# Optimization experiments

Hardware: AMD Instinct MI355X
Metric: run time of the kernel (lower is better)

Reference implementation:

```python
import jax, jax.numpy as jnp
import numpy as np

B, S, D, H, F, E = 4, 1024, 1024, 16, 4096, 8
HD = D // H  # head dim


def setup_inputs() -> dict:
    key = jax.random.key(0)
    ks = jax.random.split(key, 8)
    p = lambda k, shp: jax.random.normal(k, shp, jnp.float32) * 0.02
    return {
        "x": jax.random.normal(ks[0], (B, S, D), jnp.float32),
        "mask": jnp.ones((B, S), jnp.int32),
        "in_proj_w": p(ks[1], (3 * D, D)),
        "in_proj_b": jnp.zeros((3 * D,), jnp.float32),
        "out_proj_w": p(ks[2], (D, D)),
        "out_proj_b": jnp.zeros((D,), jnp.float32),
        "ln1_g": jnp.ones((D,), jnp.float32),
        "ln1_b": jnp.zeros((D,), jnp.float32),
        "ln2_g": jnp.ones((D,), jnp.float32),
        "ln2_b": jnp.zeros((D,), jnp.float32),
        "gate_w": p(ks[3], (E, D)),
        "gate_b": jnp.zeros((E,), jnp.float32),
        "w1": p(ks[4], (E, F, D)),
        "b1": jnp.zeros((E, F), jnp.float32),
        "w2": p(ks[5], (E, D, F)),
        "b2": jnp.zeros((E, D), jnp.float32),
    }


def _layernorm(x, g, b, eps=1e-5):
    m = x.mean(-1, keepdims=True)
    v = ((x - m) ** 2).mean(-1, keepdims=True)
    return (x - m) / jnp.sqrt(v + eps) * g + b


def _mha(x, key_pad, in_proj_w, in_proj_b, out_proj_w, out_proj_b):
    # combined QKV projection as in torch nn.MultiheadAttention
    qkv = x @ in_proj_w.T + in_proj_b  # (B,S,3D)
    q, k, v = jnp.split(qkv, 3, axis=-1)
    def heads(t):
        return t.reshape(B, S, H, HD).transpose(0, 2, 1, 3)  # (B,H,S,HD)
    q, k, v = heads(q), heads(k), heads(v)
    scores = jnp.einsum("bhqd,bhkd->bhqk", q, k) / jnp.sqrt(jnp.float32(HD))
    scores = jnp.where(key_pad[:, None, None, :], -1e30, scores)
    attn = jax.nn.softmax(scores, axis=-1)
    out = jnp.einsum("bhqk,bhkd->bhqd", attn, v)  # (B,H,S,HD)
    out = out.transpose(0, 2, 1, 3).reshape(B, S, D)
    return out @ out_proj_w.T + out_proj_b


def _moe(x, gate_w, gate_b, w1, b1, w2, b2):
    logits = x @ gate_w.T + gate_b            # (B,S,E)
    probs = jax.nn.softmax(logits, axis=-1)
    # dense all-expert FFN (faithful to original: every expert computed)
    h = jax.nn.relu(jnp.einsum("bsd,efd->bsef", x, w1) + b1)   # (B,S,E,F)
    all_out = jnp.einsum("bsef,edf->bsed", h, w2) + b2          # (B,S,E,D)
    top_vals, top_idx = jax.lax.top_k(probs, 2)                 # (B,S,2)
    weights = top_vals / (top_vals.sum(-1, keepdims=True) + 1e-9)
    sel = jnp.take_along_axis(all_out, top_idx[..., None], axis=2)  # (B,S,2,D)
    return (sel * weights[..., None]).sum(axis=2)


def reference(x, mask, in_proj_w, in_proj_b, out_proj_w, out_proj_b,
              ln1_g, ln1_b, ln2_g, ln2_b, gate_w, gate_b, w1, b1, w2, b2):
    key_pad = mask == 0  # (B,S) bool
    attn_out = _mha(x, key_pad, in_proj_w, in_proj_b, out_proj_w, out_proj_b)
    x1 = _layernorm(x + attn_out, ln1_g, ln1_b)
    ff = _moe(x1, gate_w, gate_b, w1, b1, w2, b2)
    return _layernorm(x1 + ff, ln2_g, ln2_b)
```

## Files before the change

kernel.cpp:

```cpp
#include <hip/hip_runtime.h>

typedef __attribute__((ext_vector_type(8))) short bf16x8;
typedef __attribute__((ext_vector_type(4))) float f32x4;

#define DEV __device__ __forceinline__

static constexpr int Bb = 4, Sq = 1024, Dd = 1024, Hh = 16, HDd = 64, Ff = 4096, Ee = 8;
static constexpr int Nn = Bb * Sq;
static constexpr int TD = 3 * Dd;
static constexpr int PMAX = 2 * Nn + Ee * 256;

DEV unsigned short f2bf(float x) {
  union { float f; unsigned u; } c; c.f = x;
  unsigned r = c.u + 0x7FFFu + ((c.u >> 16) & 1u);
  return (unsigned short)(r >> 16);
}

typedef const __attribute__((address_space(1))) unsigned int* gas_t;
typedef __attribute__((address_space(3))) unsigned int* las_t;
DEV void gload16(const void* g, void* l) {
  __builtin_amdgcn_global_load_lds((gas_t)g, (las_t)l, 16, 0, 0);
}

__global__ __launch_bounds__(256) void cvt_kernel(const float* __restrict__ in,
                                                  unsigned short* __restrict__ out) {
  int i = blockIdx.x * 256 + threadIdx.x;
  const float4 a = *(const float4*)(in + (size_t)i * 8);
  const float4 b = *(const float4*)(in + (size_t)i * 8 + 4);
  union { uint4 u; unsigned short s[8]; } pk;
  pk.s[0] = f2bf(a.x); pk.s[1] = f2bf(a.y); pk.s[2] = f2bf(a.z); pk.s[3] = f2bf(a.w);
  pk.s[4] = f2bf(b.x); pk.s[5] = f2bf(b.y); pk.s[6] = f2bf(b.z); pk.s[7] = f2bf(b.w);
  *(uint4*)(out + (size_t)i * 8) = pk.u;
}

template <int EPI, int TN>
__global__ __launch_bounds__(512) void gemm256(
    const unsigned short* __restrict__ A, const unsigned short* __restrict__ Bw,
    const float* __restrict__ bias, void* __restrict__ o0,
    int Ncols, int K, const int* __restrict__ poff) {
  constexpr int NW_N = TN / 64;
  constexpr int NW_M = 8 / NW_N;
  constexpr int RM = 256 / NW_M;
  constexpr int MI = RM / 16;
  constexpr int NB = TN / 64;
  constexpr int ASZ = 256 * 64;
  constexpr int BSZ = TN * 64;

  int bx, by;
  {
    const int gx = gridDim.x, nwg = gx * gridDim.y;
    int orig = blockIdx.y * gx + blockIdx.x;
    int q = nwg >> 3, r = nwg & 7;
    int xcd = orig & 7, lin = orig >> 3;
    int wg = (xcd < r ? xcd * (q + 1) : r * (q + 1) + (xcd - r) * q) + lin;
    bx = wg % gx; by = wg / gx;
  }
  const int m0 = bx * 256;
  if (m0 >= poff[Ee]) return;
  int e = 0;
#pragma unroll
  for (int k = 1; k < Ee; ++k) if (m0 >= poff[k]) e = k;
  const int n0 = by * TN;
  const unsigned short* Bptr = Bw + (size_t)e * Ncols * K;
  const float* biasptr = bias + e * Ncols;

  __shared__ __align__(128) unsigned short As[2 * ASZ];
  __shared__ __align__(128) unsigned short Bs[2 * BSZ];

  const int tid = threadIdx.x;
  const int lane = tid & 63, wid = tid >> 6;
  const int wm = wid / NW_N, wn = wid % NW_N;
  const int lr = lane & 15, lk = lane >> 4;

  const char* aSrc[4]; const char* bSrc[NB];
  int aDstOff[4], bDstOff[NB];
#pragma unroll
  for (int it = 0; it < 4; ++it) {
    int b = it * 8192 + tid * 16;
    int r = b >> 7;
    int colb = (b & 127) ^ ((r & 7) << 4);
    aSrc[it] = (const char*)(A + (size_t)(m0 + r) * K) + colb;
    aDstOff[it] = it * 8192 + wid * 1024;
  }
#pragma unroll
  for (int it = 0; it < NB; ++it) {
    int b = it * 8192 + tid * 16;
    int r = b >> 7;
    int colb = (b & 127) ^ ((r & 7) << 4);
    bSrc[it] = (const char*)(Bptr + (size_t)(n0 + r) * K) + colb;
    bDstOff[it] = it * 8192 + wid * 1024;
  }
  int aOff[2][MI], bOff[2][4];
#pragma unroll
  for (int ks = 0; ks < 2; ++ks) {
#pragma unroll
    for (int i = 0; i < MI; ++i) {
      int ra = wm * RM + i * 16 + lr;
      aOff[ks][i] = ra * 64 + (((ks * 4 + lk) ^ (ra & 7)) << 3);
    }
#pragma unroll
    for (int i = 0; i < 4; ++i) {
      int rb = wn * 64 + i * 16 + lr;
      bOff[ks][i] = rb * 64 + (((ks * 4 + lk) ^ (rb & 7)) << 3);
    }
  }

  f32x4 acc[MI][4] = {};
  const int NT = K >> 6;

  auto STAGE = [&](int t, int buf) {
#pragma unroll
    for (int it = 0; it < 4; ++it)
      gload16(aSrc[it] + (size_t)t * 128, (char*)As + buf * (ASZ * 2) + aDstOff[it]);
#pragma unroll
    for (int it = 0; it < NB; ++it)
      gload16(bSrc[it] + (size_t)t * 128, (char*)Bs + buf * (BSZ * 2) + bDstOff[it]);
  };

  STAGE(0, 0);
  for (int t = 0; t < NT; ++t) {
    __builtin_amdgcn_s_barrier();
    __builtin_amdgcn_sched_barrier(0);
    if (t + 1 < NT) {
      STAGE(t + 1, (t + 1) & 1);
      if constexpr (TN == 256) asm volatile("s_waitcnt vmcnt(8)" ::: "memory");
      else                     asm volatile("s_waitcnt vmcnt(6)" ::: "memory");
    } else {
      asm volatile("s_waitcnt vmcnt(0)" ::: "memory");
    }
    __builtin_amdgcn_sched_barrier(0);
    __builtin_amdgcn_s_barrier();
    __builtin_amdgcn_sched_barrier(0);
    const unsigned short* Ab = As + (t & 1) * ASZ;
    const unsigned short* Bb2 = Bs + (t & 1) * BSZ;
#pragma unroll
    for (int ks = 0; ks < 2; ++ks) {
      bf16x8 af[MI], bfv[4];
#pragma unroll
      for (int mi = 0; mi < MI; ++mi) af[mi] = *(const bf16x8*)&Ab[aOff[ks][mi]];
#pragma unroll
      for (int ni = 0; ni < 4; ++ni) bfv[ni] = *(const bf16x8*)&Bb2[bOff[ks][ni]];
#pragma unroll
      for (int mi = 0; mi < MI; ++mi)
#pragma unroll
        for (int ni = 0; ni < 4; ++ni)
          acc[mi][ni] = __builtin_amdgcn_mfma_f32_16x16x32_bf16(af[mi], bfv[ni], acc[mi][ni], 0, 0, 0);
    }
  }

#pragma unroll
  for (int ni = 0; ni < 4; ++ni) {
    const int col = n0 + wn * 64 + ni * 16 + lr;
    const float bv = biasptr[col];
#pragma unroll
    for (int mi = 0; mi < MI; ++mi) {
#pragma unroll
      for (int i = 0; i < 4; ++i) {
        const int grow = m0 + wm * RM + mi * 16 + lk * 4 + i;
        float v = acc[mi][ni][i] + bv;
        if constexpr (EPI == 2) {
          ((unsigned short*)o0)[(size_t)grow * Ff + col] = f2bf(fmaxf(v, 0.f));
        } else {
          ((float*)o0)[(size_t)grow * Dd + col] = v;
        }
      }
    }
  }
}

template <int EPI>
__global__ __launch_bounds__(256) void gemm_bt(
    const unsigned short* __restrict__ A, const unsigned short* __restrict__ Bw,
    const float* __restrict__ bias, void* __restrict__ o0, void* __restrict__ o1,
    void* __restrict__ o2, int M, int Ncols, int K) {
  int bx, by;
  {
    const int gx = gridDim.x, nwg = gx * gridDim.y;
    int orig = blockIdx.y * gx + blockIdx.x;
    int q = nwg >> 3, r = nwg & 7;
    int xcd = orig & 7, lin = orig >> 3;
    int wg = (xcd < r ? xcd * (q + 1) : r * (q + 1) + (xcd - r) * q) + lin;
    bx = wg % gx; by = wg / gx;
  }
  const int m0 = bx * 128;
  if (m0 >= M) return;
  const int n0 = by * 128;

  __shared__ __align__(128) unsigned short As[3 * 128 * 32];
  __shared__ __align__(128) unsigned short Bs[3 * 128 * 32];

  const int tid = threadIdx.x;
  const int lane = tid & 63, wid = tid >> 6;
  const int wm = wid >> 1, wn = wid & 1;
  const int lr = lane & 15, lk = lane >> 4;

  const char* aSrc[2]; const char* bSrc[2];
  int dOff[2];
#pragma unroll
  for (int it = 0; it < 2; ++it) {
    int b = it * 4096 + tid * 16;
    int r = b >> 6;
    int colb = (b & 63) ^ (((r >> 1) & 3) << 4);
    aSrc[it] = (const char*)(A + (size_t)(m0 + r) * K) + colb;
    bSrc[it] = (const char*)(Bw + (size_t)(n0 + r) * K) + colb;
    dOff[it] = it * 4096 + wid * 1024;
  }
  int aOff[4], bOff[4];
#pragma unroll
  for (int i = 0; i < 4; ++i) {
    int ra = wm * 64 + i * 16 + lr;
    aOff[i] = ra * 32 + ((lk ^ ((ra >> 1) & 3)) << 3);
    int rb = wn * 64 + i * 16 + lr;
    bOff[i] = rb * 32 + ((lk ^ ((rb >> 1) & 3)) << 3);
  }

  auto STAGE = [&](int t, int buf) {
#pragma unroll
    for (int it = 0; it < 2; ++it) {
      gload16(aSrc[it] + (size_t)t * 64, (char*)As + buf * 8192 + dOff[it]);
      gload16(bSrc[it] + (size_t)t * 64, (char*)Bs + buf * 8192 + dOff[it]);
    }
  };

  f32x4 acc[4][4] = {};
  const int NT = K >> 5;

  STAGE(0, 0);
  STAGE(1, 1);
  int cb = 0, sb = 2;
  for (int t = 0; t < NT; ++t) {
    if (t + 1 < NT) asm volatile("s_waitcnt vmcnt(4)" ::: "memory");
    else            asm volatile("s_waitcnt vmcnt(0)" ::: "memory");
    __builtin_amdgcn_sched_barrier(0);
    __builtin_amdgcn_s_barrier();
    __builtin_amdgcn_sched_barrier(0);
    if (t + 2 < NT) STAGE(t + 2, sb);
    const unsigned short* Ab = As + cb * 4096;
    const unsigned short* Bb2 = Bs + cb * 4096;
    bf16x8 af[4], bfv[4];
#pragma unroll
    for (int mi = 0; mi < 4; ++mi) af[mi] = *(const bf16x8*)&Ab[aOff[mi]];
#pragma unroll
    for (int ni = 0; ni < 4; ++ni) bfv[ni] = *(const bf16x8*)&Bb2[bOff[ni]];
#pragma unroll
    for (int mi = 0; mi < 4; ++mi)
#pragma unroll
      for (int ni = 0; ni < 4; ++ni)
        acc[mi][ni] = __builtin_amdgcn_mfma_f32_16x16x32_bf16(af[mi], bfv[ni], acc[mi][ni], 0, 0, 0);
    cb = (cb == 2) ? 0 : cb + 1;
    sb = (sb == 2) ? 0 : sb + 1;
  }

#pragma unroll
  for (int ni = 0; ni < 4; ++ni) {
    const int col = n0 + wn * 64 + ni * 16 + lr;
    const float bv = bias[col];
#pragma unroll
    for (int mi = 0; mi < 4; ++mi) {
#pragma unroll
      for (int i = 0; i < 4; ++i) {
        const int mloc = wm * 64 + mi * 16 + lk * 4 + i;
        float v = acc[mi][ni][i] + bv;
        if constexpr (EPI == 0) {
          int t = m0 + mloc;
          int which = col >> 10, jj = col & 1023, hh = jj >> 6, hd = jj & 63;
          int bb = t >> 10, s = t & 1023;
          unsigned short* dst = (which == 0) ? (unsigned short*)o0
                              : (which == 1) ? (unsigned short*)o1 : (unsigned short*)o2;
          dst[((size_t)(bb * Hh + hh) * Sq + s) * HDd + hd] = f2bf(v);
        } else {
          ((float*)o0)[(size_t)(m0 + mloc) * Dd + col] = v;
        }
      }
    }
  }
}

__global__ __launch_bounds__(256) void attn_kernel(
    const unsigned short* __restrict__ qb, const unsigned short* __restrict__ kb,
    const unsigned short* __restrict__ vb, const int* __restrict__ mask,
    unsigned short* __restrict__ attnb) {
  const int qt = blockIdx.x, h = blockIdx.y, b = blockIdx.z;
  const unsigned short* Q = qb + (size_t)(b * Hh + h) * Sq * HDd;
  const unsigned short* Kg = kb + (size_t)(b * Hh + h) * Sq * HDd;
  const unsigned short* Vg = vb + (size_t)(b * Hh + h) * Sq * HDd;

  __shared__ unsigned short Qs[64 * 72], Ks[64 * 72], Vt[64 * 72], Ps[64 * 72];
  __shared__ float Ssm[64 * 65];
  __shared__ float mS[64], lS[64], aS[64];
  __shared__ int mk[64];

  const int tid = threadIdx.x, lane = tid & 63, wid = tid >> 6;
  const int lr = lane & 15, lk = lane >> 4;

#pragma unroll
  for (int it = 0; it < 2; ++it) {
    int c = tid + it * 256; int r = c >> 3, kc = (c & 7) * 8;
    *(uint4*)&Qs[r * 72 + kc] = *(const uint4*)(Q + (size_t)(qt * 64 + r) * 64 + kc);
  }
  if (tid < 64) { mS[tid] = -1e30f; lS[tid] = 0.f; }

  f32x4 oacc[4] = {};

  for (int kt = 0; kt < 16; ++kt) {
    __syncthreads();
#pragma unroll
    for (int it = 0; it < 2; ++it) {
      int c = tid + it * 256; int r = c >> 3, kc = (c & 7) * 8;
      *(uint4*)&Ks[r * 72 + kc] = *(const uint4*)(Kg + (size_t)(kt * 64 + r) * 64 + kc);
    }
    {
      int kk = tid >> 2, hg = (tid & 3) * 16;
      union { uint4 u[2]; unsigned short s[16]; } tv;
      tv.u[0] = *(const uint4*)(Vg + (size_t)(kt * 64 + kk) * 64 + hg);
      tv.u[1] = *(const uint4*)(Vg + (size_t)(kt * 64 + kk) * 64 + hg + 8);
#pragma unroll
      for (int j = 0; j < 16; ++j) Vt[(hg + j) * 72 + kk] = tv.s[j];
    }
    if (tid < 64) mk[tid] = mask[b * Sq + kt * 64 + tid];
    __syncthreads();

    f32x4 sacc[4] = {};
#pragma unroll
    for (int ks = 0; ks < 2; ++ks) {
      bf16x8 aq = *(const bf16x8*)&Qs[(wid * 16 + lr) * 72 + ks * 32 + lk * 8];
#pragma unroll
      for (int ni = 0; ni < 4; ++ni) {
        bf16x8 bk = *(const bf16x8*)&Ks[(ni * 16 + lr) * 72 + ks * 32 + lk * 8];
        sacc[ni] = __builtin_amdgcn_mfma_f32_16x16x32_bf16(aq, bk, sacc[ni], 0, 0, 0);
      }
    }
#pragma unroll
    for (int ni = 0; ni < 4; ++ni)
#pragma unroll
      for (int i = 0; i < 4; ++i) {
        int r = wid * 16 + lk * 4 + i, cc = ni * 16 + lr;
        float v = sacc[ni][i] * 0.125f;
        if (mk[cc] == 0) v = -1e30f;
        Ssm[r * 65 + cc] = v;
      }
    __syncthreads();
    {
      int r = tid >> 2, cg = (tid & 3) * 16;
      float xv[16];
#pragma unroll
      for (int j = 0; j < 16; ++j) xv[j] = Ssm[r * 65 + cg + j];
      float mx = xv[0];
#pragma unroll
      for (int j = 1; j < 16; ++j) mx = fmaxf(mx, xv[j]);
      mx = fmaxf(mx, __shfl_xor(mx, 1));
      mx = fmaxf(mx, __shfl_xor(mx, 2));
      float mprev = mS[r];
      float mnew = fmaxf(mprev, mx);
      float sum = 0.f;
      union { uint4 u[2]; unsigned short s[16]; } pb;
#pragma unroll
      for (int j = 0; j < 16; ++j) {
        float pv = expf(xv[j] - mnew);
        sum += pv; pb.s[j] = f2bf(pv);
      }
      sum += __shfl_xor(sum, 1);
      sum += __shfl_xor(sum, 2);
      *(uint4*)&Ps[r * 72 + cg] = pb.u[0];
      *(uint4*)&Ps[r * 72 + cg + 8] = pb.u[1];
      if ((tid & 3) == 0) {
        float alpha = expf(mprev - mnew);
        mS[r] = mnew; aS[r] = alpha; lS[r] = lS[r] * alpha + sum;
      }
    }
    __syncthreads();
#pragma unroll
    for (int ni = 0; ni < 4; ++ni)
#pragma unroll
      for (int i = 0; i < 4; ++i)
        oacc[ni][i] *= aS[wid * 16 + lk * 4 + i];
#pragma unroll
    for (int ks = 0; ks < 2; ++ks) {
      bf16x8 ap = *(const bf16x8*)&Ps[(wid * 16 + lr) * 72 + ks * 32 + lk * 8];
#pragma unroll
      for (int ni = 0; ni < 4; ++ni) {
        bf16x8 bv = *(const bf16x8*)&Vt[(ni * 16 + lr) * 72 + ks * 32 + lk * 8];
        oacc[ni] = __builtin_amdgcn_mfma_f32_16x16x32_bf16(ap, bv, oacc[ni], 0, 0, 0);
      }
    }
  }
  __syncthreads();
#pragma unroll
  for (int ni = 0; ni < 4; ++ni)
#pragma unroll
    for (int i = 0; i < 4; ++i) {
      int r = wid * 16 + lk * 4 + i;
      int q = qt * 64 + r;
      float v = oacc[ni][i] / lS[r];
      attnb[((size_t)(b * Sq + q)) * Dd + h * 64 + ni * 16 + lr] = f2bf(v);
    }
}

__global__ __launch_bounds__(256) void ln_kernel(
    const float* __restrict__ a, const float* __restrict__ b2,
    const float* __restrict__ g, const float* __restrict__ beta,
    float* __restrict__ outf, unsigned short* __restrict__ outb) {
  const int t = blockIdx.x, tid = threadIdx.x;
  float4 v = *(const float4*)(a + (size_t)t * Dd + tid * 4);
  {
    float4 u = *(const float4*)(b2 + (size_t)t * Dd + tid * 4);
    v.x += u.x; v.y += u.y; v.z += u.z; v.w += u.w;
  }
  const int lane = tid & 63, wid = tid >> 6;
  float s = v.x + v.y + v.z + v.w;
  for (int sh = 1; sh < 64; sh <<= 1) s += __shfl_xor(s, sh);
  __shared__ float red[4], red2[4];
  if (lane == 0) red[wid] = s;
  __syncthreads();
  float mean = (red[0] + red[1] + red[2] + red[3]) * (1.f / Dd);
  float dx = v.x - mean, dy = v.y - mean, dz = v.z - mean, dw = v.w - mean;
  float q = dx * dx + dy * dy + dz * dz + dw * dw;
  for (int sh = 1; sh < 64; sh <<= 1) q += __shfl_xor(q, sh);
  if (lane == 0) red2[wid] = q;
  __syncthreads();
  float var = (red2[0] + red2[1] + red2[2] + red2[3]) * (1.f / Dd);
  float rstd = rsqrtf(var + 1e-5f);
  float4 gg = *(const float4*)(g + tid * 4);
  float4 bb = *(const float4*)(beta + tid * 4);
  float4 o;
  o.x = dx * rstd * gg.x + bb.x;
  o.y = dy * rstd * gg.y + bb.y;
  o.z = dz * rstd * gg.z + bb.z;
  o.w = dw * rstd * gg.w + bb.w;
  if (outf) *(float4*)(outf + (size_t)t * Dd + tid * 4) = o;
  if (outb) {
    ushort4 pk; pk.x = f2bf(o.x); pk.y = f2bf(o.y); pk.z = f2bf(o.z); pk.w = f2bf(o.w);
    *(ushort4*)(outb + (size_t)t * Dd + tid * 4) = pk;
  }
}

__global__ __launch_bounds__(256) void ln2_kernel(
    const float* __restrict__ x1f, const float* __restrict__ ffp,
    const int* __restrict__ inv, const float* __restrict__ wtok,
    const float* __restrict__ g, const float* __restrict__ beta,
    float* __restrict__ out) {
  const int t = blockIdx.x, tid = threadIdx.x;
  const int i0 = inv[2 * t], i1 = inv[2 * t + 1];
  const float w0 = wtok[2 * t], w1 = wtok[2 * t + 1];
  float4 v = *(const float4*)(x1f + (size_t)t * Dd + tid * 4);
  float4 u0 = *(const float4*)(ffp + (size_t)i0 * Dd + tid * 4);
  float4 u1 = *(const float4*)(ffp + (size_t)i1 * Dd + tid * 4);
  v.x += w0 * u0.x + w1 * u1.x; v.y += w0 * u0.y + w1 * u1.y;
  v.z += w0 * u0.z + w1 * u1.z; v.w += w0 * u0.w + w1 * u1.w;
  const int lane = tid & 63, wid = tid >> 6;
  float s = v.x + v.y + v.z + v.w;
  for (int sh = 1; sh < 64; sh <<= 1) s += __shfl_xor(s, sh);
  __shared__ float red[4], red2[4];
  if (lane == 0) red[wid] = s;
  __syncthreads();
  float mean = (red[0] + red[1] + red[2] + red[3]) * (1.f / Dd);
  float dx = v.x - mean, dy = v.y - mean, dz = v.z - mean, dw = v.w - mean;
  float q = dx * dx + dy * dy + dz * dz + dw * dw;
  for (int sh = 1; sh < 64; sh <<= 1) q += __shfl_xor(q, sh);
  if (lane == 0) red2[wid] = q;
  __syncthreads();
  float var = (red2[0] + red2[1] + red2[2] + red2[3]) * (1.f / Dd);
  float rstd = rsqrtf(var + 1e-5f);
  float4 gg = *(const float4*)(g + tid * 4);
  float4 bb = *(const float4*)(beta + tid * 4);
  float4 o;
  o.x = dx * rstd * gg.x + bb.x;
  o.y = dy * rstd * gg.y + bb.y;
  o.z = dz * rstd * gg.z + bb.z;
  o.w = dw * rstd * gg.w + bb.w;
  *(float4*)(out + (size_t)t * Dd + tid * 4) = o;
}

__global__ __launch_bounds__(256) void route_kernel(
    const float* __restrict__ x1f, const float* __restrict__ gw, const float* __restrict__ gb,
    int* __restrict__ cnt, int* __restrict__ tokslot, float* __restrict__ wtok) {
  __shared__ float gws[Ee * Dd];
  const int tid = threadIdx.x;
#pragma unroll
  for (int it = 0; it < 8; ++it) {
    int idx = (tid + it * 256) * 4;
    *(float4*)&gws[idx] = *(const float4*)(gw + idx);
  }
  __syncthreads();
  const int lane = tid & 63, wid = tid >> 6;
  for (int it = 0; it < 16; ++it) {
    int t = blockIdx.x * 64 + wid * 16 + it;
    float acc[Ee] = {};
    for (int i = 0; i < 16; ++i) {
      float xv = x1f[(size_t)t * Dd + i * 64 + lane];
#pragma unroll
      for (int e = 0; e < Ee; ++e) acc[e] += xv * gws[e * Dd + i * 64 + lane];
    }
#pragma unroll
    for (int e = 0; e < Ee; ++e) {
      float vv = acc[e];
      for (int sh = 1; sh < 64; sh <<= 1) vv += __shfl_xor(vv, sh);
      acc[e] = vv;
    }
    if (lane == 0) {
      float lg[Ee];
#pragma unroll
      for (int e = 0; e < Ee; ++e) lg[e] = acc[e] + gb[e];
      float m = lg[0];
#pragma unroll
      for (int e = 1; e < Ee; ++e) m = fmaxf(m, lg[e]);
      float p[Ee], ssum = 0.f;
#pragma unroll
      for (int e = 0; e < Ee; ++e) { p[e] = expf(lg[e] - m); ssum += p[e]; }
      int e0 = 0;
#pragma unroll
      for (int e = 1; e < Ee; ++e) if (p[e] > p[e0]) e0 = e;
      int e1 = -1;
#pragma unroll
      for (int e = 0; e < Ee; ++e) {
        if (e == e0) continue;
        if (e1 < 0 || p[e] > p[e1]) e1 = e;
      }
      float v0 = p[e0] / ssum, v1 = p[e1] / ssum;
      float wsum = v0 + v1 + 1e-9f;
      wtok[t * 2] = v0 / wsum; wtok[t * 2 + 1] = v1 / wsum;
      int p0 = atomicAdd(&cnt[e0], 1);
      tokslot[e0 * Nn + p0] = t * 2;
      int p1 = atomicAdd(&cnt[e1], 1);
      tokslot[e1 * Nn + p1] = t * 2 + 1;
    }
  }
}

__global__ void offsets_kernel(const int* __restrict__ cnt, int* __restrict__ poff) {
  if (threadIdx.x == 0) {
    int s = 0;
    for (int e = 0; e < Ee; ++e) { poff[e] = s; s += (cnt[e] + 255) & ~255; }
    poff[Ee] = s;
  }
}

__global__ __launch_bounds__(256) void pack_kernel(
    const unsigned short* __restrict__ x1b, const int* __restrict__ tokslot,
    const int* __restrict__ cnt, const int* __restrict__ poff,
    unsigned short* __restrict__ xg, int* __restrict__ inv) {
  const int tid = threadIdx.x;
  const int g = blockIdx.x * 8 + (tid >> 5);
  const int l = tid & 31;
  if (g >= poff[Ee]) return;
  int e = 0;
#pragma unroll
  for (int k = 1; k < Ee; ++k) if (g >= poff[k]) e = k;
  const int pos = g - poff[e];
  uint4* dst = (uint4*)(xg + (size_t)g * Dd);
  if (pos < cnt[e]) {
    const int ent = tokslot[e * Nn + pos];
    if (l == 0) inv[ent] = g;
    const uint4* src = (const uint4*)(x1b + (size_t)(ent >> 1) * Dd);
#pragma unroll
    for (int j = 0; j < 4; ++j) dst[l + j * 32] = src[l + j * 32];
  } else {
    const uint4 z = make_uint4(0, 0, 0, 0);
#pragma unroll
    for (int j = 0; j < 4; ++j) dst[l + j * 32] = z;
  }
}

extern "C" void kernel_launch(void* const* d_in, const int* in_sizes, int n_in,
                              void* d_out, int out_size, void* d_ws, size_t ws_size,
                              hipStream_t stream) {
  const float* x   = (const float*)d_in[0];
  const int*   msk = (const int*)d_in[1];
  const float* ipw = (const float*)d_in[2];
  const float* ipb = (const float*)d_in[3];
  const float* opw = (const float*)d_in[4];
  const float* opb = (const float*)d_in[5];
  const float* g1  = (const float*)d_in[6];
  const float* be1 = (const float*)d_in[7];
  const float* g2  = (const float*)d_in[8];
  const float* be2 = (const float*)d_in[9];
  const float* gw  = (const float*)d_in[10];
  const float* gb  = (const float*)d_in[11];
  const float* w1  = (const float*)d_in[12];
  const float* b1  = (const float*)d_in[13];
  const float* w2  = (const float*)d_in[14];
  const float* b2  = (const float*)d_in[15];
  float* out = (float*)d_out;

  char* p = (char*)d_ws;
  auto carve = [&](size_t bytes) { char* r = p; p += (bytes + 255) & ~(size_t)255; return r; };
  unsigned short* xb   = (unsigned short*)carve((size_t)Nn * Dd * 2);
  unsigned short* qb   = (unsigned short*)carve((size_t)Nn * Dd * 2);
  unsigned short* kb   = (unsigned short*)carve((size_t)Nn * Dd * 2);
  unsigned short* vb   = (unsigned short*)carve((size_t)Nn * Dd * 2);
  float* proj          = (float*)carve((size_t)Nn * Dd * 4);
  float* x1f           = (float*)carve((size_t)Nn * Dd * 4);
  unsigned short* x1b  = (unsigned short*)carve((size_t)Nn * Dd * 2);
  unsigned short* xg   = (unsigned short*)carve((size_t)PMAX * Dd * 2);
  float* ffp           = (float*)carve((size_t)PMAX * Dd * 4);
  unsigned short* hbuf = (unsigned short*)carve((size_t)PMAX * Ff * 2);
  unsigned short* wbuf = (unsigned short*)carve((size_t)Ee * Ff * Dd * 2);
  int* cnt             = (int*)carve(64);
  int* poff            = (int*)carve(64);
  int* tokslot         = (int*)carve((size_t)Ee * Nn * 4);
  float* wtok          = (float*)carve((size_t)2 * Nn * 4);
  int* inv             = (int*)carve((size_t)2 * Nn * 4);
  unsigned short* attnb = xb;

  cvt_kernel<<<Nn * Dd / 2048, 256, 0, stream>>>(x, xb);
  cvt_kernel<<<TD * Dd / 2048, 256, 0, stream>>>(ipw, wbuf);
  gemm_bt<0><<<dim3(Nn / 128, TD / 128), 256, 0, stream>>>(
      xb, wbuf, ipb, qb, kb, vb, Nn, TD, Dd);
  attn_kernel<<<dim3(Sq / 64, Hh, Bb), 256, 0, stream>>>(qb, kb, vb, msk, attnb);
  cvt_kernel<<<Dd * Dd / 2048, 256, 0, stream>>>(opw, wbuf);
  gemm_bt<1><<<dim3(Nn / 128, Dd / 128), 256, 0, stream>>>(
      attnb, wbuf, opb, proj, nullptr, nullptr, Nn, Dd, Dd);
  ln_kernel<<<Nn, 256, 0, stream>>>(x, proj, g1, be1, x1f, x1b);
  hipMemsetAsync(cnt, 0, 64, stream);
  route_kernel<<<Nn / 64, 256, 0, stream>>>(x1f, gw, gb, cnt, tokslot, wtok);
  offsets_kernel<<<1, 64, 0, stream>>>(cnt, poff);
  pack_kernel<<<PMAX / 8, 256, 0, stream>>>(x1b, tokslot, cnt, poff, xg, inv);
  cvt_kernel<<<Ee * Ff * Dd / 2048, 256, 0, stream>>>(w1, wbuf);
  gemm256<2, 256><<<dim3(PMAX / 256, Ff / 256), 512, 0, stream>>>(
      xg, wbuf, b1, hbuf, Ff, Dd, poff);
  cvt_kernel<<<Ee * Dd * Ff / 2048, 256, 0, stream>>>(w2, wbuf);
  gemm256<3, 128><<<dim3(PMAX / 256, Dd / 128), 512, 0, stream>>>(
      hbuf, wbuf, b2, ffp, Dd, Ff, poff);
  ln2_kernel<<<Nn, 256, 0, stream>>>(x1f, ffp, inv, wtok, g2, be2, out);
}
```

Measured before the change: 700.2 us.

## Restructure MoE GEMMs into quadrant-phased pipelines with split-K down projection

Replaces the generic grouped MoE GEMM with two specialized kernels. The up-projection tile is split into four 128x128 quadrants whose loads are interleaved with the MFMA phases, and each phase has finer vmcnt waits and raised scheduling priority around the MFMAs. The down-projection splits K in two across blockIdx.z and accumulates into a pre-zeroed output with atomicAdd, doubling the number of workgroups. The aim is better overlap of global-to-LDS loads with compute and higher occupancy, at the cost of an extra memset and float atomic traffic.

```diff
diff --git a/kernel.cpp b/kernel.cpp
--- a/kernel.cpp
+++ b/kernel.cpp
@@ -33,139 +33,291 @@
   *(uint4*)(out + (size_t)i * 8) = pk.u;
 }
 
-template <int EPI, int TN>
-__global__ __launch_bounds__(512) void gemm256(
+DEV void xcd_swz(int& bx, int& by, int gx, int gy) {
+  const int nwg = gx * gy;
+  int orig = by * gx + bx;
+  int q = nwg >> 3, r = nwg & 7;
+  int xcd = orig & 7, lin = orig >> 3;
+  int wg = (xcd < r ? xcd * (q + 1) : r * (q + 1) + (xcd - r) * q) + lin;
+  bx = wg % gx; by = wg / gx;
+}
+
+__global__ __launch_bounds__(512) void gemm8p_up(
     const unsigned short* __restrict__ A, const unsigned short* __restrict__ Bw,
-    const float* __restrict__ bias, void* __restrict__ o0,
-    int Ncols, int K, const int* __restrict__ poff) {
-  constexpr int NW_N = TN / 64;
-  constexpr int NW_M = 8 / NW_N;
-  constexpr int RM = 256 / NW_M;
-  constexpr int MI = RM / 16;
-  constexpr int NB = TN / 64;
-  constexpr int ASZ = 256 * 64;
-  constexpr int BSZ = TN * 64;
-
-  int bx, by;
-  {
-    const int gx = gridDim.x, nwg = gx * gridDim.y;
-    int orig = blockIdx.y * gx + blockIdx.x;
-    int q = nwg >> 3, r = nwg & 7;
-    int xcd = orig & 7, lin = orig >> 3;
-    int wg = (xcd < r ? xcd * (q + 1) : r * (q + 1) + (xcd - r) * q) + lin;
-    bx = wg % gx; by = wg / gx;
-  }
+    const float* __restrict__ bias, unsigned short* __restrict__ o0,
+    const int* __restrict__ poff) {
+  constexpr int K = Dd;
+  constexpr int NT = K / 64;
+  int bx = blockIdx.x, by = blockIdx.y;
+  xcd_swz(bx, by, gridDim.x, gridDim.y);
   const int m0 = bx * 256;
   if (m0 >= poff[Ee]) return;
   int e = 0;
 #pragma unroll
   for (int k = 1; k < Ee; ++k) if (m0 >= poff[k]) e = k;
-  const int n0 = by * TN;
-  const unsigned short* Bptr = Bw + (size_t)e * Ncols * K;
-  const float* biasptr = bias + e * Ncols;
-
-  __shared__ __align__(128) unsigned short As[2 * ASZ];
-  __shared__ __align__(128) unsigned short Bs[2 * BSZ];
+  const int n0 = by * 256;
+  const unsigned short* Bptr = Bw + (size_t)e * Ff * K;
+  const float* biasptr = bias + e * Ff;
+
+  __shared__ __align__(128) unsigned short As[2 * 256 * 64];
+  __shared__ __align__(128) unsigned short Bs[2 * 256 * 64];
 
   const int tid = threadIdx.x;
   const int lane = tid & 63, wid = tid >> 6;
-  const int wm = wid / NW_N, wn = wid % NW_N;
+  const int aw = wid & 1, bw = wid >> 1;
   const int lr = lane & 15, lk = lane >> 4;
 
-  const char* aSrc[4]; const char* bSrc[NB];
-  int aDstOff[4], bDstOff[NB];
-#pragma unroll
-  for (int it = 0; it < 4; ++it) {
+  const char* aS[2][2]; const char* bS[2][2]; int dOf[2];
+#pragma unroll
+  for (int it = 0; it < 2; ++it) {
     int b = it * 8192 + tid * 16;
     int r = b >> 7;
     int colb = (b & 127) ^ ((r & 7) << 4);
-    aSrc[it] = (const char*)(A + (size_t)(m0 + r) * K) + colb;
-    aDstOff[it] = it * 8192 + wid * 1024;
-  }
-#pragma unroll
-  for (int it = 0; it < NB; ++it) {
+#pragma unroll
+    for (int h = 0; h < 2; ++h) {
+      aS[h][it] = (const char*)(A + (size_t)(m0 + h * 128 + r) * K) + colb;
+      bS[h][it] = (const char*)(Bptr + (size_t)(n0 + h * 128 + r) * K) + colb;
+    }
+    dOf[it] = it * 8192 + wid * 1024;
+  }
+  int aO[2][2][4], bO[2][2][2];
+#pragma unroll
+  for (int h = 0; h < 2; ++h)
+#pragma unroll
+    for (int ks = 0; ks < 2; ++ks) {
+#pragma unroll
+      for (int mi = 0; mi < 4; ++mi) {
+        int ra = h * 128 + aw * 64 + mi * 16 + lr;
+        aO[h][ks][mi] = ra * 64 + (((ks * 4 + lk) ^ (ra & 7)) << 3);
+      }
+#pragma unroll
+      for (int ni = 0; ni < 2; ++ni) {
+        int rb = h * 128 + bw * 32 + ni * 16 + lr;
+        bO[h][ks][ni] = rb * 64 + (((ks * 4 + lk) ^ (rb & 7)) << 3);
+      }
+    }
+
+  f32x4 acc[4][4][2] = {};
+
+  auto ST_A = [&](int t, int h) {
+    int buf = t & 1;
+#pragma unroll
+    for (int it = 0; it < 2; ++it)
+      gload16(aS[h][it] + (size_t)t * 128, (char*)As + buf * 32768 + h * 16384 + dOf[it]);
+  };
+  auto ST_B = [&](int t, int h) {
+    int buf = t & 1;
+#pragma unroll
+    for (int it = 0; it < 2; ++it)
+      gload16(bS[h][it] + (size_t)t * 128, (char*)Bs + buf * 32768 + h * 16384 + dOf[it]);
+  };
+
+  ST_A(0, 0); ST_B(0, 0); ST_B(0, 1); ST_A(0, 1);
+
+  for (int t = 0; t < NT; ++t) {
+    const unsigned short* Ab = As + (t & 1) * 16384;
+    const unsigned short* Bb = Bs + (t & 1) * 16384;
+#pragma unroll
+    for (int p = 0; p < 4; ++p) {
+      const int ah = p >> 1, bh = p & 1;
+      if (t + 1 < NT) {
+        if (p == 0)      ST_A(t + 1, 0);
+        else if (p == 1) ST_B(t + 1, 0);
+        else if (p == 2) ST_B(t + 1, 1);
+        else             ST_A(t + 1, 1);
+        asm volatile("s_waitcnt vmcnt(6)" ::: "memory");
+      } else {
+        if (p == 0)      asm volatile("s_waitcnt vmcnt(4)" ::: "memory");
+        else if (p == 1) asm volatile("s_waitcnt vmcnt(2)" ::: "memory");
+        else             asm volatile("s_waitcnt vmcnt(0)" ::: "memory");
+      }
+      __builtin_amdgcn_sched_barrier(0);
+      asm volatile("s_barrier" ::: "memory");
+      __builtin_amdgcn_sched_barrier(0);
+      bf16x8 af[2][4], bf[2][2];
+#pragma unroll
+      for (int ks = 0; ks < 2; ++ks) {
+#pragma unroll
+        for (int mi = 0; mi < 4; ++mi) af[ks][mi] = *(const bf16x8*)&Ab[aO[ah][ks][mi]];
+#pragma unroll
+        for (int ni = 0; ni < 2; ++ni) bf[ks][ni] = *(const bf16x8*)&Bb[bO[bh][ks][ni]];
+      }
+      __builtin_amdgcn_s_setprio(1);
+#pragma unroll
+      for (int ks = 0; ks < 2; ++ks)
+#pragma unroll
+        for (int mi = 0; mi < 4; ++mi)
+#pragma unroll
+          for (int ni = 0; ni < 2; ++ni)
+            acc[p][mi][ni] = __builtin_amdgcn_mfma_f32_16x16x32_bf16(af[ks][mi], bf[ks][ni], acc[p][mi][ni], 0, 0, 0);
+      __builtin_amdgcn_s_setprio(0);
+    }
+  }
+
+#pragma unroll
+  for (int p = 0; p < 4; ++p)
+#pragma unroll
+    for (int ni = 0; ni < 2; ++ni) {
+      const int col = n0 + (p & 1) * 128 + bw * 32 + ni * 16 + lr;
+      const float bv = biasptr[col];
+#pragma unroll
+      for (int mi = 0; mi < 4; ++mi)
+#pragma unroll
+        for (int i = 0; i < 4; ++i) {
+          const int row = m0 + (p >> 1) * 128 + aw * 64 + mi * 16 + lk * 4 + i;
+          float v = acc[p][mi][ni][i] + bv;
+          o0[(size_t)row * Ff + col] = f2bf(fmaxf(v, 0.f));
+        }
+    }
+}
+
+__global__ __launch_bounds__(512) void gemm8p_dn(
+    const unsigned short* __restrict__ A, const unsigned short* __restrict__ Bw,
+    const float* __restrict__ bias, float* __restrict__ o0,
+    const int* __restrict__ poff) {
+  constexpr int K = Ff;
+  constexpr int NT = 32;
+  const int kh = blockIdx.z;
+  int bx = blockIdx.x, by = blockIdx.y;
+  xcd_swz(bx, by, gridDim.x, gridDim.y);
+  const int m0 = bx * 256;
+  if (m0 >= poff[Ee]) return;
+  int e = 0;
+#pragma unroll
+  for (int k = 1; k < Ee; ++k) if (m0 >= poff[k]) e = k;
+  const int n0 = by * 128;
+  const size_t kbB = (size_t)kh * 2048 * 2;
+  const unsigned short* Bptr = Bw + (size_t)e * Dd * K;
+  const float* biasptr = bias + e * Dd;
+
+  __shared__ __align__(128) unsigned short As[2 * 256 * 64];
+  __shared__ __align__(128) unsigned short Bs[2 * 128 * 64];
+
+  const int tid = threadIdx.x;
+  const int lane = tid & 63, wid = tid >> 6;
+  const int rw = wid >> 1, cw = wid & 1;
+  const int lr = lane & 15, lk = lane >> 4;
+
+  const char* aS[2][2]; const char* bS[2]; int dOf[2];
+#pragma unroll
+  for (int it = 0; it < 2; ++it) {
     int b = it * 8192 + tid * 16;
     int r = b >> 7;
     int colb = (b & 127) ^ ((r & 7) << 4);
-    bSrc[it] = (const char*)(Bptr + (size_t)(n0 + r) * K) + colb;
-    bDstOff[it] = it * 8192 + wid * 1024;
-  }
-  int aOff[2][MI], bOff[2][4];
-#pragma unroll
-  for (int ks = 0; ks < 2; ++ks) {
-#pragma unroll
-    for (int i = 0; i < MI; ++i) {
-      int ra = wm * RM + i * 16 + lr;
-      aOff[ks][i] = ra * 64 + (((ks * 4 + lk) ^ (ra & 7)) << 3);
-    }
-#pragma unroll
-    for (int i = 0; i < 4; ++i) {
-      int rb = wn * 64 + i * 16 + lr;
-      bOff[ks][i] = rb * 64 + (((ks * 4 + lk) ^ (rb & 7)) << 3);
-    }
-  }
-
-  f32x4 acc[MI][4] = {};
-  const int NT = K >> 6;
-
-  auto STAGE = [&](int t, int buf) {
-#pragma unroll
-    for (int it = 0; it < 4; ++it)
-      gload16(aSrc[it] + (size_t)t * 128, (char*)As + buf * (ASZ * 2) + aDstOff[it]);
-#pragma unroll
-    for (int it = 0; it < NB; ++it)
-      gload16(bSrc[it] + (size_t)t * 128, (char*)Bs + buf * (BSZ * 2) + bDstOff[it]);
+#pragma unroll
+    for (int h = 0; h < 2; ++h)
+      aS[h][it] = (const char*)(A + (size_t)(m0 + h * 128 + r) * K) + kbB + colb;
+    bS[it] = (const char*)(Bptr + (size_t)(n0 + r) * K) + kbB + colb;
+    dOf[it] = it * 8192 + wid * 1024;
+  }
+  int aO[2][2][2], bO[2][4];
+#pragma unroll
+  for (int h = 0; h < 2; ++h)
+#pragma unroll
+    for (int ks = 0; ks < 2; ++ks)
+#pragma unroll
+      for (int mi = 0; mi < 2; ++mi) {
+        int ra = h * 128 + rw * 32 + mi * 16 + lr;
+        aO[h][ks][mi] = ra * 64 + (((ks * 4 + lk) ^ (ra & 7)) << 3);
+      }
+#pragma unroll
+  for (int ks = 0; ks < 2; ++ks)
+#pragma unroll
+    for (int ni = 0; ni < 4; ++ni) {
+      int rb = cw * 64 + ni * 16 + lr;
+      bO[ks][ni] = rb * 64 + (((ks * 4 + lk) ^ (rb & 7)) << 3);
+    }
+
+  f32x4 acc[2][2][4] = {};
+
+  auto ST_A = [&](int t, int h) {
+    int buf = t & 1;
+#pragma unroll
+    for (int it = 0; it < 2; ++it)
+      gload16(aS[h][it] + (size_t)t * 128, (char*)As + buf * 32768 + h * 16384 + dOf[it]);
   };
-
-  STAGE(0, 0);
+  auto ST_B = [&](int t) {
+    int buf = t & 1;
+#pragma unroll
+    for (int it = 0; it < 2; ++it)
+      gload16(bS[it] + (size_t)t * 128, (char*)Bs + buf * 16384 + dOf[it]);
+  };
+
+  ST_A(0, 0); ST_B(0); ST_A(0, 1);
+
   for (int t = 0; t < NT; ++t) {
-    __builtin_amdgcn_s_barrier();
+    const unsigned short* Ab = As + (t & 1) * 16384;
+    const unsigned short* Bb = Bs + (t & 1) * 8192;
+    bf16x8 bf[2][4];
+    if (t + 1 < NT) {
+      ST_A(t + 1, 0); ST_B(t + 1);
+      asm volatile("s_waitcnt vmcnt(6)" ::: "memory");
+    } else {
+      asm volatile("s_waitcnt vmcnt(2)" ::: "memory");
+    }
     __builtin_amdgcn_sched_barrier(0);
+    asm volatile("s_barrier" ::: "memory");
+    __builtin_amdgcn_sched_barrier(0);
+    {
+      bf16x8 af[2][2];
+#pragma unroll
+      for (int ks = 0; ks < 2; ++ks) {
+#pragma unroll
+        for (int mi = 0; mi < 2; ++mi) af[ks][mi] = *(const bf16x8*)&Ab[aO[0][ks][mi]];
+#pragma unroll
+        for (int ni = 0; ni < 4; ++ni) bf[ks][ni] = *(const bf16x8*)&Bb[bO[ks][ni]];
+      }
+      __builtin_amdgcn_s_setprio(1);
+#pragma unroll
+      for (int ks = 0; ks < 2; ++ks)
+#pragma unroll
+        for (int mi = 0; mi < 2; ++mi)
+#pragma unroll
+          for (int ni = 0; ni < 4; ++ni)
+            acc[0][mi][ni] = __builtin_amdgcn_mfma_f32_16x16x32_bf16(af[ks][mi], bf[ks][ni], acc[0][mi][ni], 0, 0, 0);
+      __builtin_amdgcn_s_setprio(0);
+    }
     if (t + 1 < NT) {
-      STAGE(t + 1, (t + 1) & 1);
-      if constexpr (TN == 256) asm volatile("s_waitcnt vmcnt(8)" ::: "memory");
-      else                     asm volatile("s_waitcnt vmcnt(6)" ::: "memory");
+      ST_A(t + 1, 1);
+      asm volatile("s_waitcnt vmcnt(6)" ::: "memory");
     } else {
       asm volatile("s_waitcnt vmcnt(0)" ::: "memory");
     }
     __builtin_amdgcn_sched_barrier(0);
-    __builtin_amdgcn_s_barrier();
+    asm volatile("s_barrier" ::: "memory");
     __builtin_amdgcn_sched_barrier(0);
-    const unsigned short* Ab = As + (t & 1) * ASZ;
-    const unsigned short* Bb2 = Bs + (t & 1) * BSZ;
-#pragma unroll
-    for (int ks = 0; ks < 2; ++ks) {
-      bf16x8 af[MI], bfv[4];
-#pragma unroll
-      for (int mi = 0; mi < MI; ++mi) af[mi] = *(const bf16x8*)&Ab[aOff[ks][mi]];
-#pragma unroll
-      for (int ni = 0; ni < 4; ++ni) bfv[ni] = *(const bf16x8*)&Bb2[bOff[ks][ni]];
-#pragma unroll
-      for (int mi = 0; mi < MI; ++mi)
-#pragma unroll
-        for (int ni = 0; ni < 4; ++ni)
-          acc[mi][ni] = __builtin_amdgcn_mfma_f32_16x16x32_bf16(af[mi], bfv[ni], acc[mi][ni], 0, 0, 0);
-    }
-  }
-
-#pragma unroll
-  for (int ni = 0; ni < 4; ++ni) {
-    const int col = n0 + wn * 64 + ni * 16 + lr;
-    const float bv = biasptr[col];
-#pragma unroll
-    for (int mi = 0; mi < MI; ++mi) {
-#pragma unroll
-      for (int i = 0; i < 4; ++i) {
-        const int grow = m0 + wm * RM + mi * 16 + lk * 4 + i;
-        float v = acc[mi][ni][i] + bv;
-        if constexpr (EPI == 2) {
-          ((unsigned short*)o0)[(size_t)grow * Ff + col] = f2bf(fmaxf(v, 0.f));
-        } else {
-          ((float*)o0)[(size_t)grow * Dd + col] = v;
+    {
+      bf16x8 af[2][2];
+#pragma unroll
+      for (int ks = 0; ks < 2; ++ks)
+#pragma unroll
+        for (int mi = 0; mi < 2; ++mi) af[ks][mi] = *(const bf16x8*)&Ab[aO[1][ks][mi]];
+      __builtin_amdgcn_s_setprio(1);
+#pragma unroll
+      for (int ks = 0; ks < 2; ++ks)
+#pragma unroll
+        for (int mi = 0; mi < 2; ++mi)
+#pragma unroll
+          for (int ni = 0; ni < 4; ++ni)
+            acc[1][mi][ni] = __builtin_amdgcn_mfma_f32_16x16x32_bf16(af[ks][mi], bf[ks][ni], acc[1][mi][ni], 0, 0, 0);
+      __builtin_amdgcn_s_setprio(0);
+    }
+  }
+
+#pragma unroll
+  for (int ph = 0; ph < 2; ++ph)
+#pragma unroll
+    for (int ni = 0; ni < 4; ++ni) {
+      const int col = n0 + cw * 64 + ni * 16 + lr;
+      const float bv = (kh == 0) ? biasptr[col] : 0.f;
+#pragma unroll
+      for (int mi = 0; mi < 2; ++mi)
+#pragma unroll
+        for (int i = 0; i < 4; ++i) {
+          const int row = m0 + ph * 128 + rw * 32 + mi * 16 + lk * 4 + i;
+          atomicAdd(&o0[(size_t)row * Dd + col], acc[ph][mi][ni][i] + bv);
         }
-      }
-    }
-  }
+    }
 }
 
 template <int EPI>
@@ -173,15 +325,8 @@
     const unsigned short* __restrict__ A, const unsigned short* __restrict__ Bw,
     const float* __restrict__ bias, void* __restrict__ o0, void* __restrict__ o1,
     void* __restrict__ o2, int M, int Ncols, int K) {
-  int bx, by;
-  {
-    const int gx = gridDim.x, nwg = gx * gridDim.y;
-    int orig = blockIdx.y * gx + blockIdx.x;
-    int q = nwg >> 3, r = nwg & 7;
-    int xcd = orig & 7, lin = orig >> 3;
-    int wg = (xcd < r ? xcd * (q + 1) : r * (q + 1) + (xcd - r) * q) + lin;
-    bx = wg % gx; by = wg / gx;
-  }
+  int bx = blockIdx.x, by = blockIdx.y;
+  xcd_swz(bx, by, gridDim.x, gridDim.y);
   const int m0 = bx * 128;
   if (m0 >= M) return;
   const int n0 = by * 128;
@@ -616,10 +761,9 @@
   offsets_kernel<<<1, 64, 0, stream>>>(cnt, poff);
   pack_kernel<<<PMAX / 8, 256, 0, stream>>>(x1b, tokslot, cnt, poff, xg, inv);
   cvt_kernel<<<Ee * Ff * Dd / 2048, 256, 0, stream>>>(w1, wbuf);
-  gemm256<2, 256><<<dim3(PMAX / 256, Ff / 256), 512, 0, stream>>>(
-      xg, wbuf, b1, hbuf, Ff, Dd, poff);
+  gemm8p_up<<<dim3(PMAX / 256, Ff / 256), 512, 0, stream>>>(xg, wbuf, b1, hbuf, poff);
   cvt_kernel<<<Ee * Dd * Ff / 2048, 256, 0, stream>>>(w2, wbuf);
-  gemm256<3, 128><<<dim3(PMAX / 256, Dd / 128), 512, 0, stream>>>(
-      hbuf, wbuf, b2, ffp, Dd, Ff, poff);
+  hipMemsetAsync(ffp, 0, (size_t)PMAX * Dd * 4, stream);
+  gemm8p_dn<<<dim3(PMAX / 256, Dd / 128, 2), 512, 0, stream>>>(hbuf, wbuf, b2, ffp, poff);
   ln2_kernel<<<Nn, 256, 0, stream>>>(x1f, ffp, inv, wtok, g2, be2, out);
 }
```

Result: faster. 668.7 us (-4.5%).
